# Kernel optimization log

Hardware: AMD Instinct MI355X
Metric: run time of the kernel (lower is better)

## Reference

```python
import jax, jax.numpy as jnp
import numpy as np

D_MODEL = 2048
NUM_HEADS = 16
HEAD_DIM = D_MODEL // NUM_HEADS
BATCH = 2
SEQ = 2048


def setup_inputs() -> dict:
    key = jax.random.key(0)
    ks = jax.random.split(key, 5)
    scale = 1.0 / np.sqrt(D_MODEL)
    x = jax.random.normal(ks[0], (BATCH, SEQ, D_MODEL), dtype=jnp.float32)
    wq = jax.random.normal(ks[1], (D_MODEL, D_MODEL), dtype=jnp.float32) * scale
    wk = jax.random.normal(ks[2], (D_MODEL, D_MODEL), dtype=jnp.float32) * scale
    wv = jax.random.normal(ks[3], (D_MODEL, D_MODEL), dtype=jnp.float32) * scale
    wo = jax.random.normal(ks[4], (D_MODEL, D_MODEL), dtype=jnp.float32) * scale
    return {"x": x, "wq": wq, "wk": wk, "wv": wv, "wo": wo}


def reference(x, wq, wk, wv, wo):
    # x: [B, S, D_MODEL]; torch nn.Linear(bias=False): y = x @ W.T
    B, S, _ = x.shape

    def split_heads(t):
        # [B, S, D] -> [B, H, S, Dh]
        return t.reshape(B, S, NUM_HEADS, HEAD_DIM).transpose(0, 2, 1, 3)

    q = split_heads(x @ wq.T)
    k = split_heads(x @ wk.T)
    v = split_heads(x @ wv.T)

    # scaled dot-product attention with causal (tril) mask, single-rank path
    scores = jnp.einsum("bhqd,bhkd->bhqk", q, k) / jnp.sqrt(
        jnp.asarray(HEAD_DIM, dtype=x.dtype)
    )
    causal = jnp.tril(jnp.ones((S, S), dtype=bool))  # [S, S]
    neg_inf = jnp.asarray(jnp.finfo(scores.dtype).min, dtype=scores.dtype)
    scores = jnp.where(causal[None, None, :, :], scores, neg_inf)
    attn = jax.nn.softmax(scores, axis=-1)

    out = jnp.einsum("bhqk,bhkd->bhqd", attn, v)  # [B, H, S, Dh]
    out = out.transpose(0, 2, 1, 3).reshape(B, S, D_MODEL)
    return out @ wo.T
```

## Files before the change

kernel.cpp:

```cpp
#include <hip/hip_runtime.h>
#include <hip/hip_bf16.h>

#define D_MODEL   2048
#define NUM_HEADS 16
#define HEAD_DIM  128
#define BATCH     2
#define SEQ       2048

typedef short bf16x8 __attribute__((ext_vector_type(8)));
typedef float f32x4  __attribute__((ext_vector_type(4)));

__device__ inline short f2bf(float x) {
    __hip_bfloat16 h = __float2bfloat16(x);
    return *reinterpret_cast<short*>(&h);
}

__device__ inline void async_copy16(const void* g, void* l) {
    __builtin_amdgcn_global_load_lds(
        (const __attribute__((address_space(1))) void*)g,
        (__attribute__((address_space(3))) void*)l, 16, 0, 0);
}
__device__ inline void wait_all() { __builtin_amdgcn_s_waitcnt(0); }

__global__ __launch_bounds__(256) void f32_to_bf16(
    const float* __restrict__ src, __hip_bfloat16* __restrict__ dst, int n8) {
    const int i = blockIdx.x * 256 + threadIdx.x;
    if (i >= n8) return;
    const f32x4* p = (const f32x4*)src + (size_t)i * 2;
    f32x4 f0 = p[0], f1 = p[1];
    bf16x8 v;
#pragma unroll
    for (int j = 0; j < 4; ++j) { v[j] = f2bf(f0[j]); v[4 + j] = f2bf(f1[j]); }
    *(bf16x8*)((short*)dst + (size_t)i * 8) = v;
}

__global__ __launch_bounds__(256) void cvt5(
    const float* __restrict__ x,  __hip_bfloat16* __restrict__ xb,
    const float* __restrict__ w0, __hip_bfloat16* __restrict__ w0b,
    const float* __restrict__ w1, __hip_bfloat16* __restrict__ w1b,
    const float* __restrict__ w2, __hip_bfloat16* __restrict__ w2b,
    const float* __restrict__ w3, __hip_bfloat16* __restrict__ w3b) {
    const int b = blockIdx.x;
    const float* src; short* dst; int idx;
    if (b < 4096)       { src = x;  dst = (short*)xb;  idx = b; }
    else if (b < 6144)  { src = w0; dst = (short*)w0b; idx = b - 4096; }
    else if (b < 8192)  { src = w1; dst = (short*)w1b; idx = b - 6144; }
    else if (b < 10240) { src = w2; dst = (short*)w2b; idx = b - 8192; }
    else                { src = w3; dst = (short*)w3b; idx = b - 10240; }
    const int i = idx * 256 + threadIdx.x;
    const f32x4* p = (const f32x4*)src + (size_t)i * 2;
    f32x4 f0 = p[0], f1 = p[1];
    bf16x8 v;
#pragma unroll
    for (int j = 0; j < 4; ++j) { v[j] = f2bf(f0[j]); v[4 + j] = f2bf(f1[j]); }
    *(bf16x8*)(dst + (size_t)i * 8) = v;
}

template <bool OUT_F32>
__global__ __launch_bounds__(256) void gemm_v3(
    const __hip_bfloat16* __restrict__ A,
    const __hip_bfloat16* __restrict__ W0,
    const __hip_bfloat16* __restrict__ W1,
    const __hip_bfloat16* __restrict__ W2,
    void* __restrict__ C0, void* __restrict__ C1, void* __restrict__ C2,
    int M, int N, int K) {
    __shared__ __hip_bfloat16 As[128 * 32];
    __shared__ __hip_bfloat16 Ws[128 * 32];

    const int z = blockIdx.z;
    const __hip_bfloat16* W = (z == 0) ? W0 : (z == 1) ? W1 : W2;
    void* Cv = (z == 0) ? C0 : (z == 1) ? C1 : C2;

    const int tid  = threadIdx.x;
    const int lane = tid & 63;
    const int wv   = tid >> 6;
    const int c    = lane & 15;
    const int quad = lane >> 4;
    const int m0   = blockIdx.y * 128;
    const int n0   = blockIdx.x * 128;
    const int wm   = (wv >> 1) * 64;
    const int wn   = (wv & 1) * 64;

    f32x4 acc[4][4];
#pragma unroll
    for (int mi = 0; mi < 4; ++mi)
#pragma unroll
        for (int ni = 0; ni < 4; ++ni)
            acc[mi][ni] = (f32x4){0.f, 0.f, 0.f, 0.f};

    const int nk = K >> 5;
    for (int kb = 0; kb < nk; ++kb) {
        __syncthreads();
#pragma unroll
        for (int i = 0; i < 2; ++i) {
            const int o   = wv * 2048 + i * 1024 + lane * 16;
            const int row = o >> 6;
            const int col = (o & 63) >> 1;
            async_copy16(&A[(size_t)(m0 + row) * K + kb * 32 + col], (char*)As + o);
            async_copy16(&W[(size_t)(n0 + row) * K + kb * 32 + col], (char*)Ws + o);
        }
        wait_all();
        __syncthreads();

        bf16x8 a[4], b[4];
#pragma unroll
        for (int mi = 0; mi < 4; ++mi)
            a[mi] = *(const bf16x8*)((const short*)As + (wm + mi * 16 + c) * 32 + quad * 8);
#pragma unroll
        for (int ni = 0; ni < 4; ++ni)
            b[ni] = *(const bf16x8*)((const short*)Ws + (wn + ni * 16 + c) * 32 + quad * 8);
#pragma unroll
        for (int mi = 0; mi < 4; ++mi)
#pragma unroll
            for (int ni = 0; ni < 4; ++ni)
                acc[mi][ni] = __builtin_amdgcn_mfma_f32_16x16x32_bf16(
                    a[mi], b[ni], acc[mi][ni], 0, 0, 0);
    }

#pragma unroll
    for (int mi = 0; mi < 4; ++mi)
#pragma unroll
        for (int ni = 0; ni < 4; ++ni)
#pragma unroll
            for (int r = 0; r < 4; ++r) {
                const int m = m0 + wm + mi * 16 + quad * 4 + r;
                const int n = n0 + wn + ni * 16 + c;
                if (OUT_F32)
                    ((float*)Cv)[(size_t)m * N + n] = acc[mi][ni][r];
                else
                    ((__hip_bfloat16*)Cv)[(size_t)m * N + n] = __float2bfloat16(acc[mi][ni][r]);
            }
}

__global__ __launch_bounds__(256) void transpose2k(
    const __hip_bfloat16* __restrict__ Vin, __hip_bfloat16* __restrict__ Vout) {
    __shared__ short T[64 * 72];
    const int tid = threadIdx.x;
    const int d0  = blockIdx.x * 64;
    const int s0  = blockIdx.y * 64;
    const size_t half = (size_t)SEQ * D_MODEL;
    const short* in  = (const short*)Vin + blockIdx.z * half;
    short*       out = (short*)Vout      + blockIdx.z * half;

#pragma unroll
    for (int i = 0; i < 2; ++i) {
        const int lin = i * 256 + tid;
        const int sr  = lin >> 3;
        const int sg  = lin & 7;
        *(uint4*)&T[sr * 72 + sg * 8] =
            *(const uint4*)&in[(size_t)(s0 + sr) * D_MODEL + d0 + sg * 8];
    }
    __syncthreads();
#pragma unroll
    for (int i = 0; i < 2; ++i) {
        const int lin = i * 256 + tid;
        const int dr  = lin >> 3;
        const int sg  = lin & 7;
        bf16x8 v;
#pragma unroll
        for (int j = 0; j < 8; ++j) v[j] = T[(sg * 8 + j) * 72 + dr];
        *(uint4*)&out[(size_t)(d0 + dr) * SEQ + s0 + sg * 8] = *(uint4*)&v;
    }
}

__global__ __launch_bounds__(256) void attn_v8(
    const __hip_bfloat16* Qg,
    const __hip_bfloat16* __restrict__ Kg,
    const __hip_bfloat16* __restrict__ Vt,
    __hip_bfloat16* Og) {
    constexpr int LDP = 72;
    __shared__ short Ks[2][64 * 128];
    __shared__ short Vs[2][128 * 64];
    __shared__ __hip_bfloat16 Pl[64 * LDP];

    const int tid  = threadIdx.x;
    const int lane = tid & 63;
    const int w    = tid >> 6;
    const int c    = lane & 15;
    const int quad = lane >> 4;
    const int qlo  = blockIdx.x;
    const int qhi  = (SEQ / 64 - 1) - qlo;
    const int h    = blockIdx.y;
    const size_t half = (size_t)SEQ * D_MODEL;
    const __hip_bfloat16* Qb  = Qg + blockIdx.z * half;
    const __hip_bfloat16* Kb  = Kg + blockIdx.z * half;
    const __hip_bfloat16* Vtb = Vt + blockIdx.z * half;
    __hip_bfloat16*       Ob  = Og + blockIdx.z * half;
    const size_t base = (size_t)h * HEAD_DIM;
    const int prow0 = w * 16;
    const float scale = 0.08838834764831845f;

    for (int pass = 0; pass < 2; ++pass) {
        const int myq = pass ? qlo : qhi;
        const int q0  = myq * 64;
        const int wq0 = q0 + prow0;

        __syncthreads();

        bf16x8 qf[4];
#pragma unroll
        for (int kk = 0; kk < 4; ++kk)
            qf[kk] = *(const bf16x8*)((const short*)Qb + base +
                                      (size_t)(wq0 + c) * D_MODEL + kk * 32 + quad * 8);

        float l_run[4] = {0.f, 0.f, 0.f, 0.f};
        f32x4 o_acc[8];
#pragma unroll
        for (int dt = 0; dt < 8; ++dt) o_acc[dt] = (f32x4){0.f, 0.f, 0.f, 0.f};

#pragma unroll
        for (int i = 0; i < 4; ++i) {
            const int o = (i * 256 + tid) * 16;
            {
                const int row = o >> 8, colb = o & 255;
                const int scol = colb ^ ((row & 7) << 4);
                async_copy16((const char*)(Kb + base + (size_t)row * D_MODEL) + scol,
                             (char*)Ks[0] + o);
            }
            {
                const int row = o >> 7, colb = o & 127;
                const int scol = colb ^ ((row & 7) << 4);
                async_copy16((const char*)(Vtb + (size_t)(base + row) * SEQ) + scol,
                             (char*)Vs[0] + o);
            }
        }

        int cur = 0;
        const int nch = myq + 1;
        for (int ch = 0; ch < nch; ++ch) {
            __syncthreads();

            if (ch + 1 < nch) {
                const int key0n = (ch + 1) * 64;
#pragma unroll
                for (int i = 0; i < 4; ++i) {
                    const int o = (i * 256 + tid) * 16;
                    {
                        const int row = o >> 8, colb = o & 255;
                        const int scol = colb ^ ((row & 7) << 4);
                        async_copy16((const char*)(Kb + base + (size_t)(key0n + row) * D_MODEL) + scol,
                                     (char*)Ks[cur ^ 1] + o);
                    }
                    {
                        const int row = o >> 7, colb = o & 127;
                        const int scol = colb ^ ((row & 7) << 4);
                        async_copy16((const char*)(Vtb + (size_t)(base + row) * SEQ + key0n) + scol,
                                     (char*)Vs[cur ^ 1] + o);
                    }
                }
            }

            const int key0 = ch * 64;
            const short* Ksc = Ks[cur];
            const short* Vsc = Vs[cur];
            f32x4 s[4];
#pragma unroll
            for (int kt = 0; kt < 4; ++kt) s[kt] = (f32x4){0.f, 0.f, 0.f, 0.f};
            __builtin_amdgcn_s_setprio(1);
#pragma unroll
            for (int kk = 0; kk < 4; ++kk)
#pragma unroll
                for (int kt = 0; kt < 4; ++kt) {
                    const int r  = kt * 16 + c;
                    const int cb = (kk * 64 + quad * 16) ^ ((r & 7) << 4);
                    bf16x8 kf = *(const bf16x8*)((const char*)Ksc + r * 256 + cb);
                    s[kt] = __builtin_amdgcn_mfma_f32_16x16x32_bf16(qf[kk], kf, s[kt], 0, 0, 0);
                }
            __builtin_amdgcn_s_setprio(0);

            const bool diag = (ch == myq);
#pragma unroll
            for (int r = 0; r < 4; ++r) {
                const int qg = wq0 + quad * 4 + r;
                const int lrow = prow0 + quad * 4 + r;
                float p[4], rs = 0.f;
#pragma unroll
                for (int kt = 0; kt < 4; ++kt) {
                    float v = s[kt][r] * scale;
                    if (diag && (key0 + kt * 16 + c > qg)) v = -1e30f;
                    p[kt] = __expf(v);
                    rs += p[kt];
                }
#pragma unroll
                for (int off = 1; off < 16; off <<= 1)
                    rs += __shfl_xor(rs, off);
                l_run[r] += rs;
#pragma unroll
                for (int kt = 0; kt < 4; ++kt)
                    Pl[lrow * LDP + kt * 16 + c] = __float2bfloat16(p[kt]);
            }

#pragma unroll
            for (int kk = 0; kk < 2; ++kk) {
                bf16x8 pa = *(const bf16x8*)((const short*)Pl +
                                             (prow0 + c) * LDP + kk * 32 + quad * 8);
                __builtin_amdgcn_s_setprio(1);
#pragma unroll
                for (int dt = 0; dt < 8; ++dt) {
                    const int rv  = dt * 16 + c;
                    const int cbv = (kk * 64 + quad * 16) ^ ((rv & 7) << 4);
                    bf16x8 vb = *(const bf16x8*)((const char*)Vsc + rv * 128 + cbv);
                    o_acc[dt] = __builtin_amdgcn_mfma_f32_16x16x32_bf16(pa, vb, o_acc[dt], 0, 0, 0);
                }
                __builtin_amdgcn_s_setprio(0);
            }

            cur ^= 1;
        }

#pragma unroll
        for (int r = 0; r < 4; ++r) {
            const float inv = 1.0f / l_run[r];
            const int row = wq0 + quad * 4 + r;
#pragma unroll
            for (int dt = 0; dt < 8; ++dt)
                Ob[base + (size_t)row * D_MODEL + dt * 16 + c] =
                    __float2bfloat16(o_acc[dt][r] * inv);
        }
    }
}

template <bool A_F32, bool W_F32, bool OUT_F32>
__global__ __launch_bounds__(256) void gemm_bt(
    const void* __restrict__ Av, const void* __restrict__ Wv,
    void* __restrict__ Cv, int M, int N, int K) {
    __shared__ __hip_bfloat16 As[128 * 32];
    __shared__ __hip_bfloat16 Ws[128 * 32];
    const int tid = threadIdx.x, lane = tid & 63, wv = tid >> 6;
    const int c = lane & 15, quad = lane >> 4;
    const int m0 = blockIdx.y * 128, n0 = blockIdx.x * 128;
    const int wm = (wv >> 1) * 64, wn = (wv & 1) * 64;
    f32x4 acc[4][4];
#pragma unroll
    for (int mi = 0; mi < 4; ++mi)
#pragma unroll
        for (int ni = 0; ni < 4; ++ni) acc[mi][ni] = (f32x4){0.f, 0.f, 0.f, 0.f};
    const int nk = K >> 5;
    for (int kb = 0; kb < nk; ++kb) {
        __syncthreads();
#pragma unroll
        for (int i = 0; i < 2; ++i) {
            const int e = (i * 256 + tid) * 8;
            const int row = e >> 5, col = e & 31;
            if (A_F32) {
                const float* p = (const float*)Av + (size_t)(m0 + row) * K + kb * 32 + col;
                f32x4 f0 = *(const f32x4*)p, f1 = *(const f32x4*)(p + 4);
                bf16x8 v;
#pragma unroll
                for (int j = 0; j < 4; ++j) { v[j] = f2bf(f0[j]); v[4 + j] = f2bf(f1[j]); }
                *(bf16x8*)((short*)As + e) = v;
            } else {
                *(uint4*)((short*)As + e) =
                    *(const uint4*)((const short*)Av + (size_t)(m0 + row) * K + kb * 32 + col);
            }
            if (W_F32) {
                const float* p = (const float*)Wv + (size_t)(n0 + row) * K + kb * 32 + col;
                f32x4 f0 = *(const f32x4*)p, f1 = *(const f32x4*)(p + 4);
                bf16x8 v;
#pragma unroll
                for (int j = 0; j < 4; ++j) { v[j] = f2bf(f0[j]); v[4 + j] = f2bf(f1[j]); }
                *(bf16x8*)((short*)Ws + e) = v;
            } else {
                *(uint4*)((short*)Ws + e) =
                    *(const uint4*)((const short*)Wv + (size_t)(n0 + row) * K + kb * 32 + col);
            }
        }
        __syncthreads();
        bf16x8 a[4], b[4];
#pragma unroll
        for (int mi = 0; mi < 4; ++mi)
            a[mi] = *(const bf16x8*)((const short*)As + (wm + mi * 16 + c) * 32 + quad * 8);
#pragma unroll
        for (int ni = 0; ni < 4; ++ni)
            b[ni] = *(const bf16x8*)((const short*)Ws + (wn + ni * 16 + c) * 32 + quad * 8);
#pragma unroll
        for (int mi = 0; mi < 4; ++mi)
#pragma unroll
            for (int ni = 0; ni < 4; ++ni)
                acc[mi][ni] = __builtin_amdgcn_mfma_f32_16x16x32_bf16(a[mi], b[ni], acc[mi][ni], 0, 0, 0);
    }
#pragma unroll
    for (int mi = 0; mi < 4; ++mi)
#pragma unroll
        for (int ni = 0; ni < 4; ++ni)
#pragma unroll
            for (int r = 0; r < 4; ++r) {
                const int m = m0 + wm + mi * 16 + quad * 4 + r;
                const int n = n0 + wn + ni * 16 + c;
                if (OUT_F32) ((float*)Cv)[(size_t)m * N + n] = acc[mi][ni][r];
                else ((__hip_bfloat16*)Cv)[(size_t)m * N + n] = __float2bfloat16(acc[mi][ni][r]);
            }
}

__global__ __launch_bounds__(256) void attn_fused_v2(
    const __hip_bfloat16* Qg, const __hip_bfloat16* __restrict__ Kg,
    const __hip_bfloat16* __restrict__ Vg, __hip_bfloat16* Og) {
    constexpr int LDK = 136, LDP = 72;
    __shared__ __hip_bfloat16 Kc[64 * LDK];
    __shared__ __hip_bfloat16 Vc[64 * LDK];
    __shared__ __hip_bfloat16 Pl[64 * LDP];
    __shared__ float alpha_l[64];
    __shared__ float l_l[64];
    const int tid = threadIdx.x, lane = tid & 63, w = tid >> 6;
    const int c = lane & 15, quad = lane >> 4;
    const int qb = blockIdx.x, h = blockIdx.y;
    const size_t base = (size_t)h * HEAD_DIM;
    const int q0 = qb * 64, wq0 = q0 + w * 16, dt0 = w * 2;
    bf16x8 qf[4];
#pragma unroll
    for (int kk = 0; kk < 4; ++kk)
        qf[kk] = *(const bf16x8*)((const short*)Qg + base +
                                  (size_t)(wq0 + c) * D_MODEL + kk * 32 + quad * 8);
    float m_run[4], l_run[4];
#pragma unroll
    for (int r = 0; r < 4; ++r) { m_run[r] = -1e30f; l_run[r] = 0.f; }
    f32x4 o_acc[4][2];
#pragma unroll
    for (int qt = 0; qt < 4; ++qt)
#pragma unroll
        for (int dd = 0; dd < 2; ++dd) o_acc[qt][dd] = (f32x4){0.f, 0.f, 0.f, 0.f};
    const float scale = 0.08838834764831845f;
    const int nch = qb + 1;
    for (int ch = 0; ch < nch; ++ch) {
        const int key0 = ch * 64;
        __syncthreads();
#pragma unroll
        for (int i = 0; i < 4; ++i) {
            const int lin = i * 256 + tid;
            const int kr = lin >> 4, cg = lin & 15;
            *(uint4*)((short*)Kc + kr * LDK + cg * 8) =
                *(const uint4*)&Kg[base + (size_t)(key0 + kr) * D_MODEL + cg * 8];
            *(uint4*)((short*)Vc + kr * LDK + cg * 8) =
                *(const uint4*)&Vg[base + (size_t)(key0 + kr) * D_MODEL + cg * 8];
        }
        __syncthreads();
        f32x4 s[4];
#pragma unroll
        for (int kt = 0; kt < 4; ++kt) s[kt] = (f32x4){0.f, 0.f, 0.f, 0.f};
#pragma unroll
        for (int kk = 0; kk < 4; ++kk)
#pragma unroll
            for (int kt = 0; kt < 4; ++kt) {
                bf16x8 kb = *(const bf16x8*)((const short*)Kc + (kt * 16 + c) * LDK + kk * 32 + quad * 8);
                s[kt] = __builtin_amdgcn_mfma_f32_16x16x32_bf16(qf[kk], kb, s[kt], 0, 0, 0);
            }
#pragma unroll
        for (int r = 0; r < 4; ++r) {
            const int qg = wq0 + quad * 4 + r;
            float v[4];
#pragma unroll
            for (int kt = 0; kt < 4; ++kt) {
                v[kt] = s[kt][r] * scale;
                if (key0 + kt * 16 + c > qg) v[kt] = -1e30f;
            }
            float mx = fmaxf(fmaxf(v[0], v[1]), fmaxf(v[2], v[3]));
#pragma unroll
            for (int off = 1; off < 16; off <<= 1) mx = fmaxf(mx, __shfl_xor(mx, off));
            const float m_new = fmaxf(m_run[r], mx);
            const float al = __expf(m_run[r] - m_new);
            float p[4], rs = 0.f;
#pragma unroll
            for (int kt = 0; kt < 4; ++kt) { p[kt] = __expf(v[kt] - m_new); rs += p[kt]; }
#pragma unroll
            for (int off = 1; off < 16; off <<= 1) rs += __shfl_xor(rs, off);
            l_run[r] = l_run[r] * al + rs;
            m_run[r] = m_new;
            const int lrow = w * 16 + quad * 4 + r;
#pragma unroll
            for (int kt = 0; kt < 4; ++kt) Pl[lrow * LDP + kt * 16 + c] = __float2bfloat16(p[kt]);
            if (c == 0) alpha_l[lrow] = al;
        }
        __syncthreads();
#pragma unroll
        for (int qt = 0; qt < 4; ++qt)
#pragma unroll
            for (int r = 0; r < 4; ++r) {
                const float al = alpha_l[qt * 16 + quad * 4 + r];
                o_acc[qt][0][r] *= al;
                o_acc[qt][1][r] *= al;
            }
#pragma unroll
        for (int kk = 0; kk < 2; ++kk) {
            bf16x8 pa[4];
#pragma unroll
            for (int qt = 0; qt < 4; ++qt)
                pa[qt] = *(const bf16x8*)((const short*)Pl + (qt * 16 + c) * LDP + kk * 32 + quad * 8);
#pragma unroll
            for (int dd = 0; dd < 2; ++dd) {
                bf16x8 vb;
#pragma unroll
                for (int j = 0; j < 8; ++j)
                    vb[j] = ((const short*)Vc)[(kk * 32 + quad * 8 + j) * LDK + (dt0 + dd) * 16 + c];
#pragma unroll
                for (int qt = 0; qt < 4; ++qt)
                    o_acc[qt][dd] = __builtin_amdgcn_mfma_f32_16x16x32_bf16(pa[qt], vb, o_acc[qt][dd], 0, 0, 0);
            }
        }
    }
    if (c == 0)
#pragma unroll
        for (int r = 0; r < 4; ++r) l_l[w * 16 + quad * 4 + r] = l_run[r];
    __syncthreads();
#pragma unroll
    for (int qt = 0; qt < 4; ++qt)
#pragma unroll
        for (int r = 0; r < 4; ++r) {
            const float inv = 1.0f / l_l[qt * 16 + quad * 4 + r];
            const int row = q0 + qt * 16 + quad * 4 + r;
#pragma unroll
            for (int dd = 0; dd < 2; ++dd)
                Og[base + (size_t)row * D_MODEL + (dt0 + dd) * 16 + c] =
                    __float2bfloat16(o_acc[qt][dd][r] * inv);
        }
}

extern "C" void kernel_launch(void* const* d_in, const int* in_sizes, int n_in,
                              void* d_out, int out_size, void* d_ws, size_t ws_size,
                              hipStream_t stream) {
    const float* x  = (const float*)d_in[0];
    const float* wq = (const float*)d_in[1];
    const float* wk = (const float*)d_in[2];
    const float* wv = (const float*)d_in[3];
    const float* wo = (const float*)d_in[4];
    float* out = (float*)d_out;

    const size_t half  = (size_t)SEQ * D_MODEL;
    const size_t WELEM = (size_t)D_MODEL * D_MODEL;
    const size_t needA = (4 * WELEM + 5 * 2 * half) * 2;
    const size_t needB = (4 * WELEM + 4 * half) * 2;

    if (ws_size >= needA) {
        __hip_bfloat16* wqb = (__hip_bfloat16*)d_ws;
        __hip_bfloat16* wkb = wqb + WELEM;
        __hip_bfloat16* wvb = wkb + WELEM;
        __hip_bfloat16* wob = wvb + WELEM;
        __hip_bfloat16* xb  = wob + WELEM;
        __hip_bfloat16* Q   = xb + 2 * half;
        __hip_bfloat16* Kf  = Q  + 2 * half;
        __hip_bfloat16* Vf  = Kf + 2 * half;
        __hip_bfloat16* Vt  = xb;

        cvt5<<<12288, 256, 0, stream>>>(x, xb, wq, wqb, wk, wkb, wv, wvb, wo, wob);

        gemm_v3<false><<<dim3(16, 32, 3), 256, 0, stream>>>(
            xb, wqb, wkb, wvb, Q, Kf, Vf, 4096, D_MODEL, D_MODEL);
        transpose2k<<<dim3(32, 32, 2), 256, 0, stream>>>(Vf, Vt);
        attn_v8<<<dim3(16, 16, 2), 256, 0, stream>>>(Q, Kf, Vt, Q);
        gemm_v3<true><<<dim3(16, 32, 1), 256, 0, stream>>>(
            Q, wob, wob, wob, out, out, out, 4096, D_MODEL, D_MODEL);
    } else if (ws_size >= needB) {
        __hip_bfloat16* wqb = (__hip_bfloat16*)d_ws;
        __hip_bfloat16* wkb = wqb + WELEM;
        __hip_bfloat16* wvb = wkb + WELEM;
        __hip_bfloat16* wob = wvb + WELEM;
        __hip_bfloat16* xbb = wob + WELEM;
        __hip_bfloat16* Qb  = xbb + half;
        __hip_bfloat16* Kb  = Qb + half;
        __hip_bfloat16* Vb  = Kb + half;
        __hip_bfloat16* Vtb = xbb;

        f32_to_bf16<<<2048, 256, 0, stream>>>(wq, wqb, (int)(WELEM / 8));
        f32_to_bf16<<<2048, 256, 0, stream>>>(wk, wkb, (int)(WELEM / 8));
        f32_to_bf16<<<2048, 256, 0, stream>>>(wv, wvb, (int)(WELEM / 8));
        f32_to_bf16<<<2048, 256, 0, stream>>>(wo, wob, (int)(WELEM / 8));
        for (int b = 0; b < BATCH; ++b) {
            f32_to_bf16<<<2048, 256, 0, stream>>>(x + b * half, xbb, (int)(half / 8));
            gemm_v3<false><<<dim3(16, 16, 3), 256, 0, stream>>>(
                xbb, wqb, wkb, wvb, Qb, Kb, Vb, 2048, D_MODEL, D_MODEL);
            transpose2k<<<dim3(32, 32, 1), 256, 0, stream>>>(Vb, Vtb);
            attn_v8<<<dim3(16, 16, 1), 256, 0, stream>>>(Qb, Kb, Vtb, Qb);
            gemm_v3<true><<<dim3(16, 16, 1), 256, 0, stream>>>(
                Qb, wob, wob, wob, out + b * half, out, out, 2048, D_MODEL, D_MODEL);
        }
    } else {
        __hip_bfloat16* Qb = (__hip_bfloat16*)d_ws;
        __hip_bfloat16* Kb = Qb + half;
        __hip_bfloat16* Vb = Kb + half;
        dim3 gg(16, 16);
        dim3 ga(32, 16);
        for (int b = 0; b < BATCH; ++b) {
            const float* xbp = x + b * half;
            gemm_bt<true, true, false><<<gg, 256, 0, stream>>>(xbp, wq, Qb, 2048, D_MODEL, D_MODEL);
            gemm_bt<true, true, false><<<gg, 256, 0, stream>>>(xbp, wk, Kb, 2048, D_MODEL, D_MODEL);
            gemm_bt<true, true, false><<<gg, 256, 0, stream>>>(xbp, wv, Vb, 2048, D_MODEL, D_MODEL);
            attn_fused_v2<<<ga, 256, 0, stream>>>(Qb, Kb, Vb, Qb);
            gemm_bt<false, true, true><<<gg, 256, 0, stream>>>(Qb, wo, out + b * half, 2048, D_MODEL, D_MODEL);
        }
    }
}
```

Baseline: 423.7 us.

## Double-buffer GEMM LDS tiles with swizzled layout and workgroup remapping

Replaces the projection GEMM with a version that uses a K-tile of 64 and two LDS buffers. The next tile is prefetched with async global-to-LDS copies while MFMAs run on the current tile. LDS rows are XOR-swizzled to cut bank conflicts on the bf16x8 fragment reads, workgroup IDs are remapped in groups of 8 for better L2 reuse, and s_setprio is raised around the MFMA bursts. This doubles LDS per block, which may lower occupancy, and it relies on __syncthreads waiting for the outstanding async loads.

```diff
diff --git a/kernel.cpp b/kernel.cpp
--- a/kernel.cpp
+++ b/kernel.cpp
@@ -57,27 +57,34 @@
 }
 
 template <bool OUT_F32>
-__global__ __launch_bounds__(256) void gemm_v3(
+__global__ __launch_bounds__(256) void gemm_v4(
     const __hip_bfloat16* __restrict__ A,
     const __hip_bfloat16* __restrict__ W0,
     const __hip_bfloat16* __restrict__ W1,
     const __hip_bfloat16* __restrict__ W2,
     void* __restrict__ C0, void* __restrict__ C1, void* __restrict__ C2,
     int M, int N, int K) {
-    __shared__ __hip_bfloat16 As[128 * 32];
-    __shared__ __hip_bfloat16 Ws[128 * 32];
+    __shared__ short As[2][128 * 64];
+    __shared__ short Ws[2][128 * 64];
 
     const int z = blockIdx.z;
     const __hip_bfloat16* W = (z == 0) ? W0 : (z == 1) ? W1 : W2;
     void* Cv = (z == 0) ? C0 : (z == 1) ? C1 : C2;
+
+    const int gx  = gridDim.x;
+    const int nwg = gx * gridDim.y;
+    const int wg  = blockIdx.y * gx + blockIdx.x;
+    const int swz = (wg & 7) * (nwg >> 3) + (wg >> 3);
+    const int bx  = swz % gx;
+    const int by  = swz / gx;
 
     const int tid  = threadIdx.x;
     const int lane = tid & 63;
     const int wv   = tid >> 6;
     const int c    = lane & 15;
     const int quad = lane >> 4;
-    const int m0   = blockIdx.y * 128;
-    const int n0   = blockIdx.x * 128;
+    const int m0   = by * 128;
+    const int n0   = bx * 128;
     const int wm   = (wv >> 1) * 64;
     const int wn   = (wv & 1) * 64;
 
@@ -88,33 +95,67 @@
         for (int ni = 0; ni < 4; ++ni)
             acc[mi][ni] = (f32x4){0.f, 0.f, 0.f, 0.f};
 
-    const int nk = K >> 5;
-    for (int kb = 0; kb < nk; ++kb) {
+    const char* ga[4];
+    const char* gw[4];
+    int lo[4];
+#pragma unroll
+    for (int i = 0; i < 4; ++i) {
+        const int o   = (i * 256 + tid) * 16;
+        const int row = o >> 7;
+        const int sc  = (o & 127) ^ ((row & 7) << 4);
+        ga[i] = (const char*)(A + (size_t)(m0 + row) * K) + sc;
+        gw[i] = (const char*)(W + (size_t)(n0 + row) * K) + sc;
+        lo[i] = o;
+    }
+
+    const int nt = K >> 6;
+
+#pragma unroll
+    for (int i = 0; i < 4; ++i) {
+        async_copy16(ga[i], (char*)As[0] + lo[i]);
+        async_copy16(gw[i], (char*)Ws[0] + lo[i]);
+    }
+    __syncthreads();
+
+    int cur = 0;
+    for (int t = 0; t < nt; ++t) {
+        if (t + 1 < nt) {
+            const size_t kb = (size_t)(t + 1) << 7;
+#pragma unroll
+            for (int i = 0; i < 4; ++i) {
+                async_copy16(ga[i] + kb, (char*)As[cur ^ 1] + lo[i]);
+                async_copy16(gw[i] + kb, (char*)Ws[cur ^ 1] + lo[i]);
+            }
+        }
+
+        const short* Asc = As[cur];
+        const short* Wsc = Ws[cur];
+#pragma unroll
+        for (int ks = 0; ks < 2; ++ks) {
+            bf16x8 a[4], b[4];
+#pragma unroll
+            for (int mi = 0; mi < 4; ++mi) {
+                const int r = wm + mi * 16 + c;
+                a[mi] = *(const bf16x8*)((const char*)Asc + r * 128 +
+                                         ((ks * 64 + quad * 16) ^ ((r & 7) << 4)));
+            }
+#pragma unroll
+            for (int ni = 0; ni < 4; ++ni) {
+                const int r = wn + ni * 16 + c;
+                b[ni] = *(const bf16x8*)((const char*)Wsc + r * 128 +
+                                         ((ks * 64 + quad * 16) ^ ((r & 7) << 4)));
+            }
+            __builtin_amdgcn_s_setprio(1);
+#pragma unroll
+            for (int mi = 0; mi < 4; ++mi)
+#pragma unroll
+                for (int ni = 0; ni < 4; ++ni)
+                    acc[mi][ni] = __builtin_amdgcn_mfma_f32_16x16x32_bf16(
+                        a[mi], b[ni], acc[mi][ni], 0, 0, 0);
+            __builtin_amdgcn_s_setprio(0);
+        }
         __syncthreads();
-#pragma unroll
-        for (int i = 0; i < 2; ++i) {
-            const int o   = wv * 2048 + i * 1024 + lane * 16;
-            const int row = o >> 6;
-            const int col = (o & 63) >> 1;
-            async_copy16(&A[(size_t)(m0 + row) * K + kb * 32 + col], (char*)As + o);
-            async_copy16(&W[(size_t)(n0 + row) * K + kb * 32 + col], (char*)Ws + o);
-        }
-        wait_all();
-        __syncthreads();
-
-        bf16x8 a[4], b[4];
-#pragma unroll
-        for (int mi = 0; mi < 4; ++mi)
-            a[mi] = *(const bf16x8*)((const short*)As + (wm + mi * 16 + c) * 32 + quad * 8);
-#pragma unroll
-        for (int ni = 0; ni < 4; ++ni)
-            b[ni] = *(const bf16x8*)((const short*)Ws + (wn + ni * 16 + c) * 32 + quad * 8);
-#pragma unroll
-        for (int mi = 0; mi < 4; ++mi)
-#pragma unroll
-            for (int ni = 0; ni < 4; ++ni)
-                acc[mi][ni] = __builtin_amdgcn_mfma_f32_16x16x32_bf16(
-                    a[mi], b[ni], acc[mi][ni], 0, 0, 0);
+        cur ^= 1;
     }
 
 #pragma unroll
@@ -542,11 +583,11 @@
 
         cvt5<<<12288, 256, 0, stream>>>(x, xb, wq, wqb, wk, wkb, wv, wvb, wo, wob);
 
-        gemm_v3<false><<<dim3(16, 32, 3), 256, 0, stream>>>(
+        gemm_v4<false><<<dim3(16, 32, 3), 256, 0, stream>>>(
             xb, wqb, wkb, wvb, Q, Kf, Vf, 4096, D_MODEL, D_MODEL);
         transpose2k<<<dim3(32, 32, 2), 256, 0, stream>>>(Vf, Vt);
         attn_v8<<<dim3(16, 16, 2), 256, 0, stream>>>(Q, Kf, Vt, Q);
-        gemm_v3<true><<<dim3(16, 32, 1), 256, 0, stream>>>(
+        gemm_v4<true><<<dim3(16, 32, 1), 256, 0, stream>>>(
             Q, wob, wob, wob, out, out, out, 4096, D_MODEL, D_MODEL);
     } else if (ws_size >= needB) {
         __hip_bfloat16* wqb = (__hip_bfloat16*)d_ws;
@@ -565,11 +606,11 @@
         f32_to_bf16<<<2048, 256, 0, stream>>>(wo, wob, (int)(WELEM / 8));
         for (int b = 0; b < BATCH; ++b) {
             f32_to_bf16<<<2048, 256, 0, stream>>>(x + b * half, xbb, (int)(half / 8));
-            gemm_v3<false><<<dim3(16, 16, 3), 256, 0, stream>>>(
+            gemm_v4<false><<<dim3(16, 16, 3), 256, 0, stream>>>(
                 xbb, wqb, wkb, wvb, Qb, Kb, Vb, 2048, D_MODEL, D_MODEL);
             transpose2k<<<dim3(32, 32, 1), 256, 0, stream>>>(Vb, Vtb);
             attn_v8<<<dim3(16, 16, 1), 256, 0, stream>>>(Qb, Kb, Vtb, Qb);
-            gemm_v3<true><<<dim3(16, 16, 1), 256, 0, stream>>>(
+            gemm_v4<true><<<dim3(16, 16, 1), 256, 0, stream>>>(
                 Qb, wob, wob, wob, out + b * half, out, out, 2048, D_MODEL, D_MODEL);
         }
     } else {
```

Result: faster. 375.7 us (-11.3%).
